# Performance work log

Measured on AMD Instinct MI355X. Metric: run time of the kernel, lower is better.

Reference implementation:

```python
import jax, jax.numpy as jnp
import numpy as np

N_NODES = 50000
N_EDGES = 800000
DIM = 128
N_LAYERS = 3
N_GRAPHS = 64
NEG_SLOPE = 0.2


def setup_inputs() -> dict:
    key = jax.random.key(0)
    ks = jax.random.split(key, 9)
    x = jax.random.normal(ks[0], (N_NODES, DIM), dtype=jnp.float32)
    edge_index = jax.random.randint(ks[1], (2, N_EDGES), 0, N_NODES, dtype=jnp.int32)
    batch = jnp.sort(jax.random.randint(ks[2], (N_NODES,), 0, N_GRAPHS, dtype=jnp.int32))
    Ws = jax.random.normal(ks[3], (N_LAYERS, DIM, DIM), dtype=jnp.float32) / np.sqrt(DIM)
    att_src = jax.random.normal(ks[4], (N_LAYERS, DIM), dtype=jnp.float32) * 0.1
    att_dst = jax.random.normal(ks[5], (N_LAYERS, DIM), dtype=jnp.float32) * 0.1
    biases = jnp.zeros((N_LAYERS, DIM), dtype=jnp.float32)
    Wf = jax.random.normal(ks[6], (DIM, 1), dtype=jnp.float32) / np.sqrt(DIM)
    bf = jnp.zeros((1,), dtype=jnp.float32)
    return {"x": x, "edge_index": edge_index, "batch": batch, "Ws": Ws,
            "att_src": att_src, "att_dst": att_dst, "biases": biases,
            "Wf": Wf, "bf": bf}


def _gat_layer(x, src, dst, W, a_src, a_dst, b, n_nodes):
    # PyG GATConv, heads=1: linear transform, per-edge attention, softmax over
    # edges incoming to each dst node, scatter-add aggregation, bias.
    h = x @ W                                        # [N, H]
    alpha = jax.nn.leaky_relu(
        (h * a_src).sum(-1)[src] + (h * a_dst).sum(-1)[dst], NEG_SLOPE)  # [E]
    m = jax.ops.segment_max(alpha, dst, num_segments=n_nodes)
    e = jnp.exp(alpha - m[dst])
    s = jax.ops.segment_sum(e, dst, num_segments=n_nodes)
    w = e / (s[dst] + 1e-16)                         # softmax per dst-neighborhood
    out = jax.ops.segment_sum(w[:, None] * h[src], dst, num_segments=n_nodes)
    return out + b


def reference(x, edge_index, batch, Ws, att_src, att_dst, biases, Wf, bf):
    n_nodes = x.shape[0]
    loop = jnp.arange(n_nodes, dtype=edge_index.dtype)   # add_self_loops=True
    src = jnp.concatenate([edge_index[0], loop])
    dst = jnp.concatenate([edge_index[1], loop])
    for l in range(N_LAYERS):
        x = _gat_layer(x, src, dst, Ws[l], att_src[l], att_dst[l], biases[l], n_nodes)
        x = jax.nn.relu(x)
    pooled = jax.ops.segment_sum(x, batch, num_segments=N_GRAPHS)  # global_add_pool
    y = (pooled @ Wf + bf).squeeze(-1)               # [N_GRAPHS]
    return y
```

## Files before the change

### kernel.cpp

```cpp
#include <hip/hip_runtime.h>
#include <hip/hip_bf16.h>

#define N_NODES 50000
#define DIM 128
#define N_GRAPHS 64
#define E_RAW 800000
#define E_TOT 850000
#define NSLOT 1000000
#define E_CAP 1200000
#define NEG_SLOPE 0.2f

typedef unsigned int uint;
typedef unsigned short ushort;
typedef float v2f __attribute__((ext_vector_type(2)));
typedef short bf16x8 __attribute__((ext_vector_type(8)));
typedef float f32x4 __attribute__((ext_vector_type(4)));

__device__ __forceinline__ int pi_pos(int p) {
    return (p >> 3) + 32 * ((p >> 1) & 3) + 16 * (p & 1);
}

__device__ __forceinline__ ushort f2bf(float f) {
    uint u = __float_as_uint(f);
    u += 0x7fffu + ((u >> 16) & 1u);
    return (ushort)(u >> 16);
}

__global__ void init_kernel(int* deg, int* fillc, float* pooled) {
    int i = blockIdx.x * blockDim.x + threadIdx.x;
    if (i < N_NODES) { deg[i] = 0; fillc[i] = 0; }
    if (i < N_GRAPHS * DIM) pooled[i] = 0.f;
}

__global__ void csr_init_kernel(int* __restrict__ csr_src) {
    int i = blockIdx.x * blockDim.x + threadIdx.x;
    if (i < NSLOT / 4) ((int4*)csr_src)[i] = make_int4(-1, -1, -1, -1);
}

__global__ void x2bf_kernel(const float* __restrict__ x, ushort* __restrict__ xb) {
    int i = blockIdx.x * blockDim.x + threadIdx.x;
    if (i >= N_NODES * DIM / 4) return;
    float4 v = ((const float4*)x)[i];
    ushort4 o;
    o.x = f2bf(v.x); o.y = f2bf(v.y); o.z = f2bf(v.z); o.w = f2bf(v.w);
    ((ushort4*)xb)[i] = o;
}

__global__ void wprep_kernel(const float* __restrict__ Ws, ushort* __restrict__ Wfrag) {
    int t = blockIdx.x * blockDim.x + threadIdx.x;
    if (t >= 3 * 32 * 64) return;
    int l = t >> 11;
    int rem = t & 2047;
    int chunk = rem >> 6, lane = rem & 63;
    int ks = chunk >> 3, nt = chunk & 7;
    int cc = lane & 15, gg = lane >> 4;
    const float* W = Ws + (size_t)l * DIM * DIM;
    ushort o[8];
#pragma unroll
    for (int j = 0; j < 8; ++j) {
        int kp = ks * 32 + gg * 8 + j;
        int kl = (l == 0) ? kp : pi_pos(kp);
        o[j] = f2bf(W[kl * DIM + nt * 16 + cc]);
    }
#pragma unroll
    for (int j = 0; j < 8; ++j) Wfrag[(size_t)t * 8 + j] = o[j];
}

__global__ void count_kernel(const int* __restrict__ ei, int* __restrict__ deg) {
    int e = blockIdx.x * blockDim.x + threadIdx.x;
    if (e >= E_TOT) return;
    int dst = (e < E_RAW) ? ei[E_RAW + e] : (e - E_RAW);
    atomicAdd(&deg[dst], 1);
}

__global__ void scan1_kernel(const int* __restrict__ deg, int* __restrict__ excl,
                             int* __restrict__ blksum, int n) {
    __shared__ int lds[256];
    int t = threadIdx.x;
    int i = blockIdx.x * 256 + t;
    int v = (i < n) ? ((deg[i] + 3) & ~3) : 0;
    lds[t] = v;
    __syncthreads();
    int incl = v;
    for (int off = 1; off < 256; off <<= 1) {
        int y = (t >= off) ? lds[t - off] : 0;
        __syncthreads();
        incl += y;
        lds[t] = incl;
        __syncthreads();
    }
    if (i < n) excl[i] = incl - v;
    if (t == 255) blksum[blockIdx.x] = incl;
}

__global__ void scan2_kernel(int* __restrict__ blksum, int* __restrict__ row_ptr, int nblk) {
    __shared__ int lds[256];
    int t = threadIdx.x;
    int v = (t < nblk) ? blksum[t] : 0;
    lds[t] = v;
    __syncthreads();
    int incl = v;
    for (int off = 1; off < 256; off <<= 1) {
        int y = (t >= off) ? lds[t - off] : 0;
        __syncthreads();
        incl += y;
        lds[t] = incl;
        __syncthreads();
    }
    if (t < nblk) blksum[t] = incl - v;
    if (t == nblk - 1) row_ptr[N_NODES] = incl;
}

__global__ void scan3_kernel(int* __restrict__ row_ptr, const int* __restrict__ blksum, int n) {
    int i = blockIdx.x * blockDim.x + threadIdx.x;
    if (i < n) row_ptr[i] += blksum[i >> 8];
}

__global__ void fill_kernel(const int* __restrict__ ei, const int* __restrict__ row_ptr,
                            int* __restrict__ fillc, int* __restrict__ csr_src,
                            int* __restrict__ csr_dst) {
    int e = blockIdx.x * blockDim.x + threadIdx.x;
    if (e >= E_TOT) return;
    int src, dst;
    if (e < E_RAW) { src = ei[e]; dst = ei[E_RAW + e]; }
    else           { src = dst = e - E_RAW; }
    int slot = row_ptr[dst] + atomicAdd(&fillc[dst], 1);
    csr_src[slot] = src;
    csr_dst[slot] = dst;
}

__global__ __launch_bounds__(256) void gemm_mfma_kernel(
    const ushort* __restrict__ Xb, const ushort* __restrict__ Wfrag,
    const float* __restrict__ asrc, const float* __restrict__ adst,
    uint* __restrict__ Hb, float* __restrict__ s1, float* __restrict__ s2, int nrows) {
    int wv = threadIdx.x >> 6;
    int lane = threadIdx.x & 63;
    int c = lane & 15, g = lane >> 4;
    int row0 = blockIdx.x * 64 + wv * 16;

    int arow = row0 + c;
    if (arow >= nrows) arow = nrows - 1;
    const ushort* xrow = Xb + (size_t)arow * DIM;

    f32x4 acc[8];
#pragma unroll
    for (int nt = 0; nt < 8; ++nt) acc[nt] = (f32x4)(0.f);

#pragma unroll
    for (int ks = 0; ks < 4; ++ks) {
        bf16x8 afrag = *(const bf16x8*)(xrow + ks * 32 + g * 8);
#pragma unroll
        for (int nt = 0; nt < 8; ++nt) {
            bf16x8 bfrag = *(const bf16x8*)(Wfrag + ((size_t)(ks * 8 + nt) * 64 + lane) * 8);
            acc[nt] = __builtin_amdgcn_mfma_f32_16x16x32_bf16(afrag, bfrag, acc[nt], 0, 0, 0);
        }
    }

    float a1[8], a2[8];
#pragma unroll
    for (int nt = 0; nt < 8; ++nt) { a1[nt] = asrc[c + 16 * nt]; a2[nt] = adst[c + 16 * nt]; }

#pragma unroll
    for (int r = 0; r < 4; ++r) {
        int outrow = row0 + g * 4 + r;
        bool valid = outrow < nrows;
        if (valid) {
            int w0 = __builtin_amdgcn_cvt_pk_fp8_f32(acc[0][r], acc[1][r], 0, false);
            w0     = __builtin_amdgcn_cvt_pk_fp8_f32(acc[2][r], acc[3][r], w0, true);
            int w1 = __builtin_amdgcn_cvt_pk_fp8_f32(acc[4][r], acc[5][r], 0, false);
            w1     = __builtin_amdgcn_cvt_pk_fp8_f32(acc[6][r], acc[7][r], w1, true);
            *(uint2*)&Hb[(size_t)outrow * 32 + c * 2] = make_uint2((uint)w0, (uint)w1);
        }
        float p1 = 0.f, p2 = 0.f;
#pragma unroll
        for (int nt = 0; nt < 8; ++nt) {
            p1 = fmaf(acc[nt][r], a1[nt], p1);
            p2 = fmaf(acc[nt][r], a2[nt], p2);
        }
#pragma unroll
        for (int m = 1; m < 16; m <<= 1) { p1 += __shfl_xor(p1, m); p2 += __shfl_xor(p2, m); }
        if (c == 0 && valid) { s1[outrow] = p1; s2[outrow] = p2; }
    }
}

__global__ __launch_bounds__(256) void ew_kernel(
    const int* __restrict__ csr_src, const int* __restrict__ csr_dst,
    const float* __restrict__ s1, const float* __restrict__ s2,
    float* __restrict__ w) {
    int slot = blockIdx.x * blockDim.x + threadIdx.x;
    if (slot >= NSLOT) return;
    int sv = csr_src[slot];
    float wv = 0.f;
    if (sv >= 0) {
        int dv = csr_dst[slot];
        float al = s1[sv] + s2[dv];
        al = fmaxf(al, NEG_SLOPE * al);
        wv = __expf(al);
    }
    w[slot] = wv;
}

__global__ __launch_bounds__(256) void agg_kernel(
    const uint* __restrict__ Hb, const int* __restrict__ csr_src,
    const int* __restrict__ row_ptr, const float* __restrict__ w,
    const float* __restrict__ bias,
    ushort* __restrict__ Xout, const int* __restrict__ batch,
    float* __restrict__ pooled, int pool_flag, int ngroups) {
    int gw = (blockIdx.x * blockDim.x + threadIdx.x) >> 6;
    int lane = threadIdx.x & 63;
    if (gw >= ngroups) return;
    int node0 = gw * 8;
    int q = lane & 31;
    int h = lane >> 5;

    int4 rpa = *(const int4*)&row_ptr[node0];
    int4 rpb = *(const int4*)&row_ptr[node0 + 4];
    int rp8 = row_ptr[node0 + 8];
    int rp[9] = {rpa.x, rpa.y, rpa.z, rpa.w, rpb.x, rpb.y, rpb.z, rpb.w, rp8};

    int p0 = 4 * q + 2 * h;
    float2 b2;
    b2.x = bias[pi_pos(p0)];
    b2.y = bias[pi_pos(p0) + 16];

    int ba[8] = {0, 0, 0, 0, 0, 0, 0, 0};
    if (pool_flag) {
        int4 bqa = *(const int4*)&batch[node0];
        int4 bqb = *(const int4*)&batch[node0 + 4];
        ba[0] = bqa.x; ba[1] = bqa.y; ba[2] = bqa.z; ba[3] = bqa.w;
        ba[4] = bqb.x; ba[5] = bqb.y; ba[6] = bqb.z; ba[7] = bqb.w;
    }

#pragma unroll
    for (int k = 0; k < 8; ++k) {
        int beg = rp[k], end = rp[k + 1];
        float acc0 = 0.f, acc1 = 0.f, acc2 = 0.f, acc3 = 0.f, ws = 0.f;

        for (int s = beg; s < end; s += 8) {
            int4 a = *(const int4*)&csr_src[s];
            float4 wa = *(const float4*)&w[s];
            bool vb = (s + 4) < end;
            int4 b = vb ? *(const int4*)&csr_src[s + 4] : make_int4(-1, -1, -1, -1);
            float4 wb = vb ? *(const float4*)&w[s + 4] : make_float4(0.f, 0.f, 0.f, 0.f);
            int sn[8] = {a.x, a.y, a.z, a.w, b.x, b.y, b.z, b.w};
            float wv[8] = {wa.x, wa.y, wa.z, wa.w, wb.x, wb.y, wb.z, wb.w};
#pragma unroll
            for (int p2 = 0; p2 < 4; ++p2) {
                int r0 = sn[2 * p2];     r0 = (r0 < 0) ? 0 : r0;
                int r1 = sn[2 * p2 + 1]; r1 = (r1 < 0) ? 0 : r1;
                int rsel = h ? r1 : r0;
                float wsel = h ? wv[2 * p2 + 1] : wv[2 * p2];
                uint hv = Hb[(size_t)rsel * 32 + q];
                v2f f0 = __builtin_amdgcn_cvt_pk_f32_fp8((int)hv, false);
                v2f f1 = __builtin_amdgcn_cvt_pk_f32_fp8((int)hv, true);
                acc0 = fmaf(wsel, f0.x, acc0);
                acc1 = fmaf(wsel, f0.y, acc1);
                acc2 = fmaf(wsel, f1.x, acc2);
                acc3 = fmaf(wsel, f1.y, acc3);
                ws += wsel;
            }
        }

        acc0 += __shfl_xor(acc0, 32);
        acc1 += __shfl_xor(acc1, 32);
        acc2 += __shfl_xor(acc2, 32);
        acc3 += __shfl_xor(acc3, 32);
        ws   += __shfl_xor(ws, 32);
        float inv = 1.f / (ws + 1e-16f);
        float vx = h ? acc2 : acc0;
        float vy = h ? acc3 : acc1;
        vx = fmaxf(fmaf(vx, inv, b2.x), 0.f);
        vy = fmaxf(fmaf(vy, inv, b2.y), 0.f);

        if (pool_flag) {
            atomicAdd(&pooled[ba[k] * DIM + p0], vx);
            atomicAdd(&pooled[ba[k] * DIM + p0 + 1], vy);
        } else {
            ushort2 hb;
            hb.x = f2bf(vx);
            hb.y = f2bf(vy);
            ((ushort2*)Xout)[(size_t)(node0 + k) * 64 + (p0 >> 1)] = hb;
        }
    }
}

__global__ void final_kernel(const float* __restrict__ pooled, const float* __restrict__ Wf,
                             const float* __restrict__ bf, float* __restrict__ y) {
    int wid = (blockIdx.x * blockDim.x + threadIdx.x) >> 6;
    int lane = threadIdx.x & 63;
    if (wid >= N_GRAPHS) return;
    float2 p = *(const float2*)&pooled[wid * DIM + 2 * lane];
    int cc = lane >> 2, ii = lane & 3;
    float wx = Wf[cc + 32 * ii];
    float wy = Wf[cc + 32 * ii + 16];
    float v = p.x * wx + p.y * wy;
    for (int off = 32; off; off >>= 1) v += __shfl_down(v, off);
    if (lane == 0) y[wid] = v + bf[0];
}

extern "C" void kernel_launch(void* const* d_in, const int* in_sizes, int n_in,
                              void* d_out, int out_size, void* d_ws, size_t ws_size,
                              hipStream_t stream) {
    const float* x       = (const float*)d_in[0];
    const int*   ei      = (const int*)d_in[1];
    const int*   batch   = (const int*)d_in[2];
    const float* Ws      = (const float*)d_in[3];
    const float* att_src = (const float*)d_in[4];
    const float* att_dst = (const float*)d_in[5];
    const float* biases  = (const float*)d_in[6];
    const float* Wf      = (const float*)d_in[7];
    const float* bf      = (const float*)d_in[8];
    float* y = (float*)d_out;

    char* p = (char*)d_ws;
    auto alloc = [&](size_t bytes) -> void* {
        void* r = (void*)p;
        p += (bytes + 255) & ~(size_t)255;
        return r;
    };
    ushort* xC     = (ushort*)alloc((size_t)(N_NODES + 64) * DIM * 2);
    ushort* xA     = (ushort*)alloc((size_t)(N_NODES + 64) * DIM * 2);
    uint*   Hb     = (uint*)alloc((size_t)N_NODES * 32 * 4);
    ushort* Wfrag  = (ushort*)alloc((size_t)3 * 32 * 64 * 8 * 2);
    int*   csr_src = (int*)alloc((size_t)E_CAP * 4);
    int*   csr_dst = (int*)alloc((size_t)E_CAP * 4);
    float* wbuf    = (float*)alloc((size_t)E_CAP * 4);
    int*   deg     = (int*)alloc((size_t)N_NODES * 4);
    int*   fillc   = (int*)alloc((size_t)N_NODES * 4);
    int*   row_ptr = (int*)alloc((size_t)(N_NODES + 16) * 4);
    int*   blksum  = (int*)alloc(256 * 4);
    float* s1      = (float*)alloc((size_t)N_NODES * 4);
    float* s2      = (float*)alloc((size_t)(N_NODES + 8) * 4);
    float* pooled  = (float*)alloc((size_t)N_GRAPHS * DIM * 4);

    const int BN = 256;
    const int gN   = (N_NODES + BN - 1) / BN;
    const int gE   = (E_TOT + BN - 1) / BN;
    const int ngroups = N_NODES / 8;
    const int gAGG = (ngroups * 64 + BN - 1) / BN;
    const int nblk = gN;
    const int gCVT = (N_NODES * DIM / 4 + BN - 1) / BN;
    const int gGEMM = (N_NODES + 63) / 64;
    const int gEW  = (NSLOT + BN - 1) / BN;
    const int gCI  = (NSLOT / 4 + BN - 1) / BN;

    init_kernel<<<gN, BN, 0, stream>>>(deg, fillc, pooled);
    csr_init_kernel<<<gCI, BN, 0, stream>>>(csr_src);
    x2bf_kernel<<<gCVT, BN, 0, stream>>>(x, xC);
    wprep_kernel<<<(3 * 32 * 64 + BN - 1) / BN, BN, 0, stream>>>(Ws, Wfrag);
    count_kernel<<<gE, BN, 0, stream>>>(ei, deg);
    scan1_kernel<<<nblk, BN, 0, stream>>>(deg, row_ptr, blksum, N_NODES);
    scan2_kernel<<<1, BN, 0, stream>>>(blksum, row_ptr, nblk);
    scan3_kernel<<<gN, BN, 0, stream>>>(row_ptr, blksum, N_NODES);
    fill_kernel<<<gE, BN, 0, stream>>>(ei, row_ptr, fillc, csr_src, csr_dst);

    const ushort* xin = xC;
    ushort* xout = xA;
    for (int l = 0; l < 3; ++l) {
        const ushort* Wf_l = Wfrag + (size_t)l * 32 * 64 * 8;
        const float* as = att_src + (size_t)l * DIM;
        const float* ad = att_dst + (size_t)l * DIM;
        const float* b  = biases + (size_t)l * DIM;

        gemm_mfma_kernel<<<gGEMM, BN, 0, stream>>>(xin, Wf_l, as, ad, Hb, s1, s2, N_NODES);
        ew_kernel<<<gEW, BN, 0, stream>>>(csr_src, csr_dst, s1, s2, wbuf);
        agg_kernel<<<gAGG, BN, 0, stream>>>(Hb, csr_src, row_ptr, wbuf, b,
                                            xout, batch, pooled,
                                            (l == 2) ? 1 : 0, ngroups);
        xin = xout;
        xout = (l == 0) ? xC : xA;
    }

    final_kernel<<<(N_GRAPHS * 64 + BN - 1) / BN, BN, 0, stream>>>(pooled, Wf, bf, y);
    (void)ws_size; (void)n_in; (void)in_sizes; (void)out_size;
}
```

Before: 379.2 us.

## Pack CSR src/dst into 16-bit pairs, vectorise edge weights, shrink agg groups

Replaces the separate csr_src and csr_dst int arrays with one uint array holding src in the low 16 bits and dst in the high 16 bits, using a 0xFFFF dst sentinel for padding. The edge-weight kernel now processes four slots per thread with vector loads and stores, and the aggregation kernel assigns 4 nodes per wavefront instead of 8, with a scalarised group index. The intent is to cut CSR memory traffic and improve load balance and parallelism in aggregation. The packing relies on node count fitting in 16 bits.

```diff
diff --git a/kernel.cpp b/kernel.cpp
--- a/kernel.cpp
+++ b/kernel.cpp
@@ -9,6 +9,7 @@
 #define NSLOT 1000000
 #define E_CAP 1200000
 #define NEG_SLOPE 0.2f
+#define PAD_SENT 0xFFFF0000u
 
 typedef unsigned int uint;
 typedef unsigned short ushort;
@@ -32,9 +33,9 @@
     if (i < N_GRAPHS * DIM) pooled[i] = 0.f;
 }
 
-__global__ void csr_init_kernel(int* __restrict__ csr_src) {
-    int i = blockIdx.x * blockDim.x + threadIdx.x;
-    if (i < NSLOT / 4) ((int4*)csr_src)[i] = make_int4(-1, -1, -1, -1);
+__global__ void csr_init_kernel(uint* __restrict__ csr) {
+    int i = blockIdx.x * blockDim.x + threadIdx.x;
+    if (i < NSLOT / 4) ((uint4*)csr)[i] = make_uint4(PAD_SENT, PAD_SENT, PAD_SENT, PAD_SENT);
 }
 
 __global__ void x2bf_kernel(const float* __restrict__ x, ushort* __restrict__ xb) {
@@ -117,16 +118,14 @@
 }
 
 __global__ void fill_kernel(const int* __restrict__ ei, const int* __restrict__ row_ptr,
-                            int* __restrict__ fillc, int* __restrict__ csr_src,
-                            int* __restrict__ csr_dst) {
+                            int* __restrict__ fillc, uint* __restrict__ csr) {
     int e = blockIdx.x * blockDim.x + threadIdx.x;
     if (e >= E_TOT) return;
     int src, dst;
     if (e < E_RAW) { src = ei[e]; dst = ei[E_RAW + e]; }
     else           { src = dst = e - E_RAW; }
     int slot = row_ptr[dst] + atomicAdd(&fillc[dst], 1);
-    csr_src[slot] = src;
-    csr_dst[slot] = dst;
+    csr[slot] = (uint)src | ((uint)dst << 16);
 }
 
 __global__ __launch_bounds__(256) void gemm_mfma_kernel(
@@ -184,73 +183,79 @@
 }
 
 __global__ __launch_bounds__(256) void ew_kernel(
-    const int* __restrict__ csr_src, const int* __restrict__ csr_dst,
-    const float* __restrict__ s1, const float* __restrict__ s2,
-    float* __restrict__ w) {
-    int slot = blockIdx.x * blockDim.x + threadIdx.x;
-    if (slot >= NSLOT) return;
-    int sv = csr_src[slot];
-    float wv = 0.f;
-    if (sv >= 0) {
-        int dv = csr_dst[slot];
-        float al = s1[sv] + s2[dv];
-        al = fmaxf(al, NEG_SLOPE * al);
-        wv = __expf(al);
-    }
-    w[slot] = wv;
+    const uint* __restrict__ csr, const float* __restrict__ s1,
+    const float* __restrict__ s2, float* __restrict__ w) {
+    int i = blockIdx.x * blockDim.x + threadIdx.x;
+    if (i >= NSLOT / 4) return;
+    uint4 e = ((const uint4*)csr)[i];
+    uint ev[4] = {e.x, e.y, e.z, e.w};
+    float ov[4];
+#pragma unroll
+    for (int j = 0; j < 4; ++j) {
+        uint dv = ev[j] >> 16;
+        uint sv = ev[j] & 0xFFFFu;
+        float wv = 0.f;
+        if (dv != 0xFFFFu) {
+            float al = s1[sv] + s2[dv];
+            al = fmaxf(al, NEG_SLOPE * al);
+            wv = __expf(al);
+        }
+        ov[j] = wv;
+    }
+    float4 o;
+    o.x = ov[0]; o.y = ov[1]; o.z = ov[2]; o.w = ov[3];
+    ((float4*)w)[i] = o;
 }
 
 __global__ __launch_bounds__(256) void agg_kernel(
-    const uint* __restrict__ Hb, const int* __restrict__ csr_src,
+    const uint* __restrict__ Hb, const uint* __restrict__ csr,
     const int* __restrict__ row_ptr, const float* __restrict__ w,
     const float* __restrict__ bias,
     ushort* __restrict__ Xout, const int* __restrict__ batch,
     float* __restrict__ pooled, int pool_flag, int ngroups) {
     int gw = (blockIdx.x * blockDim.x + threadIdx.x) >> 6;
+    gw = __builtin_amdgcn_readfirstlane(gw);
+    if (gw >= ngroups) return;
     int lane = threadIdx.x & 63;
-    if (gw >= ngroups) return;
-    int node0 = gw * 8;
+    int node0 = gw * 4;
     int q = lane & 31;
     int h = lane >> 5;
 
     int4 rpa = *(const int4*)&row_ptr[node0];
-    int4 rpb = *(const int4*)&row_ptr[node0 + 4];
-    int rp8 = row_ptr[node0 + 8];
-    int rp[9] = {rpa.x, rpa.y, rpa.z, rpa.w, rpb.x, rpb.y, rpb.z, rpb.w, rp8};
+    int rp4 = row_ptr[node0 + 4];
+    int rp[5] = {rpa.x, rpa.y, rpa.z, rpa.w, rp4};
 
     int p0 = 4 * q + 2 * h;
     float2 b2;
     b2.x = bias[pi_pos(p0)];
     b2.y = bias[pi_pos(p0) + 16];
 
-    int ba[8] = {0, 0, 0, 0, 0, 0, 0, 0};
+    int ba[4] = {0, 0, 0, 0};
     if (pool_flag) {
-        int4 bqa = *(const int4*)&batch[node0];
-        int4 bqb = *(const int4*)&batch[node0 + 4];
-        ba[0] = bqa.x; ba[1] = bqa.y; ba[2] = bqa.z; ba[3] = bqa.w;
-        ba[4] = bqb.x; ba[5] = bqb.y; ba[6] = bqb.z; ba[7] = bqb.w;
-    }
-
-#pragma unroll
-    for (int k = 0; k < 8; ++k) {
+        int4 bq = *(const int4*)&batch[node0];
+        ba[0] = bq.x; ba[1] = bq.y; ba[2] = bq.z; ba[3] = bq.w;
+    }
+
+#pragma unroll
+    for (int k = 0; k < 4; ++k) {
         int beg = rp[k], end = rp[k + 1];
         float acc0 = 0.f, acc1 = 0.f, acc2 = 0.f, acc3 = 0.f, ws = 0.f;
 
         for (int s = beg; s < end; s += 8) {
-            int4 a = *(const int4*)&csr_src[s];
+            uint4 a = *(const uint4*)&csr[s];
             float4 wa = *(const float4*)&w[s];
             bool vb = (s + 4) < end;
-            int4 b = vb ? *(const int4*)&csr_src[s + 4] : make_int4(-1, -1, -1, -1);
+            uint4 b = vb ? *(const uint4*)&csr[s + 4]
+                         : make_uint4(PAD_SENT, PAD_SENT, PAD_SENT, PAD_SENT);
             float4 wb = vb ? *(const float4*)&w[s + 4] : make_float4(0.f, 0.f, 0.f, 0.f);
-            int sn[8] = {a.x, a.y, a.z, a.w, b.x, b.y, b.z, b.w};
+            uint sn[8] = {a.x, a.y, a.z, a.w, b.x, b.y, b.z, b.w};
             float wv[8] = {wa.x, wa.y, wa.z, wa.w, wb.x, wb.y, wb.z, wb.w};
 #pragma unroll
             for (int p2 = 0; p2 < 4; ++p2) {
-                int r0 = sn[2 * p2];     r0 = (r0 < 0) ? 0 : r0;
-                int r1 = sn[2 * p2 + 1]; r1 = (r1 < 0) ? 0 : r1;
-                int rsel = h ? r1 : r0;
+                uint esel = h ? sn[2 * p2 + 1] : sn[2 * p2];
                 float wsel = h ? wv[2 * p2 + 1] : wv[2 * p2];
-                uint hv = Hb[(size_t)rsel * 32 + q];
+                uint rsel = esel & 0xFFFFu;
+                uint hv = Hb[rsel * 32u + (uint)q];
                 v2f f0 = __builtin_amdgcn_cvt_pk_f32_fp8((int)hv, false);
                 v2f f1 = __builtin_amdgcn_cvt_pk_f32_fp8((int)hv, true);
                 acc0 = fmaf(wsel, f0.x, acc0);
@@ -322,8 +327,7 @@
     ushort* xA     = (ushort*)alloc((size_t)(N_NODES + 64) * DIM * 2);
     uint*   Hb     = (uint*)alloc((size_t)N_NODES * 32 * 4);
     ushort* Wfrag  = (ushort*)alloc((size_t)3 * 32 * 64 * 8 * 2);
-    int*   csr_src = (int*)alloc((size_t)E_CAP * 4);
-    int*   csr_dst = (int*)alloc((size_t)E_CAP * 4);
+    uint*  csr     = (uint*)alloc((size_t)E_CAP * 4);
     float* wbuf    = (float*)alloc((size_t)E_CAP * 4);
     int*   deg     = (int*)alloc((size_t)N_NODES * 4);
     int*   fillc   = (int*)alloc((size_t)N_NODES * 4);
@@ -336,23 +340,23 @@
     const int BN = 256;
     const int gN   = (N_NODES + BN - 1) / BN;
     const int gE   = (E_TOT + BN - 1) / BN;
-    const int ngroups = N_NODES / 8;
+    const int ngroups = N_NODES / 4;
     const int gAGG = (ngroups * 64 + BN - 1) / BN;
     const int nblk = gN;
     const int gCVT = (N_NODES * DIM / 4 + BN - 1) / BN;
     const int gGEMM = (N_NODES + 63) / 64;
-    const int gEW  = (NSLOT + BN - 1) / BN;
+    const int gEW  = (NSLOT / 4 + BN - 1) / BN;
     const int gCI  = (NSLOT / 4 + BN - 1) / BN;
 
     init_kernel<<<gN, BN, 0, stream>>>(deg, fillc, pooled);
-    csr_init_kernel<<<gCI, BN, 0, stream>>>(csr_src);
+    csr_init_kernel<<<gCI, BN, 0, stream>>>(csr);
     x2bf_kernel<<<gCVT, BN, 0, stream>>>(x, xC);
     wprep_kernel<<<(3 * 32 * 64 + BN - 1) / BN, BN, 0, stream>>>(Ws, Wfrag);
     count_kernel<<<gE, BN, 0, stream>>>(ei, deg);
     scan1_kernel<<<nblk, BN, 0, stream>>>(deg, row_ptr, blksum, N_NODES);
     scan2_kernel<<<1, BN, 0, stream>>>(blksum, row_ptr, nblk);
     scan3_kernel<<<gN, BN, 0, stream>>>(row_ptr, blksum, N_NODES);
-    fill_kernel<<<gE, BN, 0, stream>>>(ei, row_ptr, fillc, csr_src, csr_dst);
+    fill_kernel<<<gE, BN, 0, stream>>>(ei, row_ptr, fillc, csr);
 
     const ushort* xin = xC;
     ushort* xout = xA;
@@ -363,8 +367,8 @@
         const float* b  = biases + (size_t)l * DIM;
 
         gemm_mfma_kernel<<<gGEMM, BN, 0, stream>>>(xin, Wf_l, as, ad, Hb, s1, s2, N_NODES);
-        ew_kernel<<<gEW, BN, 0, stream>>>(csr_src, csr_dst, s1, s2, wbuf);
-        agg_kernel<<<gAGG, BN, 0, stream>>>(Hb, csr_src, row_ptr, wbuf, b,
+        ew_kernel<<<gEW, BN, 0, stream>>>(csr, s1, s2, wbuf);
+        agg_kernel<<<gAGG, BN, 0, stream>>>(Hb, csr, row_ptr, wbuf, b,
                                             xout, batch, pooled,
                                             (l == 2) ? 1 : 0, ngroups);
         xin = xout;
```

Result: slower. 498.9 us (+31.6%).
